# Optimization experiments

Hardware: AMD Instinct MI355X
Metric: run time of the kernel (lower is better)

The kernel has to match this reference:

```python
import jax, jax.numpy as jnp
import numpy as np

EXPERT_NUM = 8
SEQ_LEN = 4096
FREQ_LEN = SEQ_LEN // 2 + 1


def setup_inputs() -> dict:
    key = jax.random.key(0)
    ks = jax.random.split(key, 6)
    B, C = 32, 8
    x = jax.random.normal(ks[0], (B, C, SEQ_LEN), dtype=jnp.float32)
    raw = jax.random.uniform(ks[1], (EXPERT_NUM - 1,), dtype=jnp.float32)
    s1 = 1.0 / np.sqrt(FREQ_LEN)
    W1 = jax.random.uniform(ks[2], (FREQ_LEN, FREQ_LEN), jnp.float32, -s1, s1)
    b1 = jax.random.uniform(ks[3], (FREQ_LEN,), jnp.float32, -s1, s1)
    W2 = jax.random.uniform(ks[4], (EXPERT_NUM, FREQ_LEN), jnp.float32, -s1, s1)
    b2 = jax.random.uniform(ks[5], (EXPERT_NUM,), jnp.float32, -s1, s1)
    return {"x": x, "raw": raw, "W1": W1, "b1": b1, "W2": W2, "b2": b2}


def reference(x, raw, W1, b1, W2, b2):
    # instance norm over seq dim (unbiased variance, like torch.var default)
    x_mean = jnp.mean(x, axis=2, keepdims=True)
    xc = x - x_mean
    n = x.shape[2]
    x_var = jnp.sum(xc * xc, axis=2, keepdims=True) / (n - 1) + 1e-5
    xn = xc / jnp.sqrt(x_var)

    freq_x = jnp.fft.rfft(xn, axis=-1)            # [B, C, F] complex
    F_ = freq_x.shape[-1]

    # sorted sigmoid boundaries -> integer band edges (non-differentiable cast)
    b = jnp.sort(jax.nn.sigmoid(raw))
    boundaries = jnp.concatenate([jnp.zeros(1, x.dtype), b, jnp.ones(1, x.dtype)])
    idx = jnp.floor(jax.lax.stop_gradient(boundaries) * F_).astype(jnp.int32)
    idx = idx.at[-1].set(F_)

    # band-pass masks for all experts at once: [E, F]
    fpos = jnp.arange(F_)
    mask = (fpos[None, :] >= idx[:-1, None]) & (fpos[None, :] < idx[1:, None])

    # per-expert frequency components: [B, E, C, F]
    comp = freq_x[:, None, :, :] * mask[None, :, None, :].astype(freq_x.dtype)
    expert_outputs = jnp.fft.irfft(comp, n=SEQ_LEN, axis=-1)  # [B, E, C, L]

    # gating on channel-averaged magnitude spectrum
    gating_input = jnp.mean(jnp.abs(freq_x), axis=1)          # [B, F]
    h = jax.nn.relu(gating_input @ W1.T + b1)
    gating_scores = jax.nn.softmax(h @ W2.T + b2, axis=-1)    # [B, E]

    # gated combine in frequency domain, then single iFFT
    gate_c = gating_scores.astype(freq_x.dtype)
    combined_freq = jnp.einsum('becf,be->bcf', comp, gate_c)
    combined = jnp.fft.irfft(combined_freq, n=SEQ_LEN, axis=-1)
    combined = combined * jnp.sqrt(x_var) + x_mean
    return combined, boundaries, gating_scores, expert_outputs
```

## Files before the change

kernel.cpp:

```cpp
#include <hip/hip_runtime.h>
#include <hip/hip_bf16.h>


using cplx = float2;
typedef float nfloat2 __attribute__((ext_vector_type(2)));

static constexpr int BB = 32, CCH = 8, LL = 4096, FF = 2049, EE = 8;

static constexpr size_t WS_FREQ  = 0;
static constexpr size_t WS_MEAN  = WS_FREQ + (size_t)BB * CCH * FF * 2;
static constexpr size_t WS_SIGMA = WS_MEAN + 256;
static constexpr size_t WS_GI    = WS_SIGMA + 256;
static constexpr size_t WS_H     = WS_GI + (size_t)BB * FF;
static constexpr size_t WS_IDX   = WS_H + (size_t)BB * FF;
static constexpr size_t WS_EOF   = WS_IDX + 16;
static constexpr size_t WS_LOGIT = WS_EOF + 2049;
static constexpr size_t WS_W2048 = WS_LOGIT + 256;
static constexpr size_t WS_U     = WS_W2048 + 4096;

static constexpr size_t OUT_COMB = 0;
static constexpr size_t OUT_BND  = (size_t)BB * CCH * LL;
static constexpr size_t OUT_GATE = OUT_BND + 9;
static constexpr size_t OUT_EXP  = OUT_GATE + (size_t)BB * EE;

#define PHI(i) ((i) + ((i) >> 5))
__device__ __forceinline__ int scat(int n) {
  return ((n & 3) << 9) | (((n >> 2) & 7) << 6) | (((n >> 5) & 7) << 3) | (n >> 8);
}

template <bool INV>
__device__ __forceinline__ void dft8(float* zr, float* zi) {
  const float C = 0.70710678118654752f;
  float s0r = zr[0] + zr[4], s0i = zi[0] + zi[4];
  float d0r = zr[0] - zr[4], d0i = zi[0] - zi[4];
  float s1r = zr[2] + zr[6], s1i = zi[2] + zi[6];
  float d1r = zr[2] - zr[6], d1i = zi[2] - zi[6];
  float E0r = s0r + s1r, E0i = s0i + s1i;
  float E2r = s0r - s1r, E2i = s0i - s1i;
  float E1r, E1i, E3r, E3i;
  if (!INV) { E1r = d0r + d1i; E1i = d0i - d1r; E3r = d0r - d1i; E3i = d0i + d1r; }
  else      { E1r = d0r - d1i; E1i = d0i + d1r; E3r = d0r + d1i; E3i = d0i - d1r; }
  float t0r = zr[1] + zr[5], t0i = zi[1] + zi[5];
  float e0r = zr[1] - zr[5], e0i = zi[1] - zi[5];
  float t1r = zr[3] + zr[7], t1i = zi[3] + zi[7];
  float e1r = zr[3] - zr[7], e1i = zi[3] - zi[7];
  float O0r = t0r + t1r, O0i = t0i + t1i;
  float O2r = t0r - t1r, O2i = t0i - t1i;
  float O1r, O1i, O3r, O3i;
  if (!INV) { O1r = e0r + e1i; O1i = e0i - e1r; O3r = e0r - e1i; O3i = e0i + e1r; }
  else      { O1r = e0r - e1i; O1i = e0i + e1r; O3r = e0r + e1i; O3i = e0i - e1r; }
  float w1r, w1i, w2r, w2i, w3r, w3i;
  if (!INV) {
    w1r = C * (O1r + O1i); w1i = C * (O1i - O1r);
    w2r = O2i;             w2i = -O2r;
    w3r = C * (O3i - O3r); w3i = -C * (O3r + O3i);
  } else {
    w1r = C * (O1r - O1i); w1i = C * (O1i + O1r);
    w2r = -O2i;            w2i = O2r;
    w3r = -C * (O3r + O3i); w3i = C * (O3r - O3i);
  }
  zr[0] = E0r + O0r; zi[0] = E0i + O0i;
  zr[4] = E0r - O0r; zi[4] = E0i - O0i;
  zr[1] = E1r + w1r; zi[1] = E1i + w1i;
  zr[5] = E1r - w1r; zi[5] = E1i - w1i;
  zr[2] = E2r + w2r; zi[2] = E2i + w2i;
  zr[6] = E2r - w2r; zi[6] = E2i - w2i;
  zr[3] = E3r + w3r; zi[3] = E3i + w3i;
  zr[7] = E3r - w3r; zi[7] = E3i - w3i;
}

template <bool INV>
__device__ __forceinline__ void dft4(float* zr, float* zi) {
  float s0r = zr[0] + zr[2], s0i = zi[0] + zi[2];
  float d0r = zr[0] - zr[2], d0i = zi[0] - zi[2];
  float s1r = zr[1] + zr[3], s1i = zi[1] + zi[3];
  float d1r = zr[1] - zr[3], d1i = zi[1] - zi[3];
  zr[0] = s0r + s1r; zi[0] = s0i + s1i;
  zr[2] = s0r - s1r; zi[2] = s0i - s1i;
  if (!INV) { zr[1] = d0r + d1i; zi[1] = d0i - d1r; zr[3] = d0r - d1i; zi[3] = d0i + d1r; }
  else      { zr[1] = d0r - d1i; zi[1] = d0i + d1r; zr[3] = d0r + d1i; zi[3] = d0i - d1r; }
}

template <bool INV>
__device__ void fftr8(float* ZR, float* ZI, const cplx* __restrict__ W, int t) {
  float zr[8], zi[8];
  {
    int base = 8 * t;
#pragma unroll
    for (int m = 0; m < 8; ++m) { int i = PHI(base + m); zr[m] = ZR[i]; zi[m] = ZI[i]; }
    dft8<INV>(zr, zi);
#pragma unroll
    for (int m = 0; m < 8; ++m) { int i = PHI(base + m); ZR[i] = zr[m]; ZI[i] = zi[m]; }
  }
  __syncthreads();
  {
    int g = t & 31, p = t >> 5;
    int base = 64 * g + p;
#pragma unroll
    for (int m = 0; m < 8; ++m) { int i = PHI(base + 8 * m); zr[m] = ZR[i]; zi[m] = ZI[i]; }
#pragma unroll
    for (int m = 1; m < 8; ++m) {
      cplx w = W[32 * m * p];
      float wi = INV ? -w.y : w.y;
      float xr = zr[m] * w.x - zi[m] * wi;
      float xi = zr[m] * wi + zi[m] * w.x;
      zr[m] = xr; zi[m] = xi;
    }
    dft8<INV>(zr, zi);
#pragma unroll
    for (int m = 0; m < 8; ++m) { int i = PHI(base + 8 * m); ZR[i] = zr[m]; ZI[i] = zi[m]; }
  }
  __syncthreads();
  {
    int g = t & 3, p = t >> 2;
    int base = 512 * g + p;
#pragma unroll
    for (int m = 0; m < 8; ++m) { int i = PHI(base + 64 * m); zr[m] = ZR[i]; zi[m] = ZI[i]; }
#pragma unroll
    for (int m = 1; m < 8; ++m) {
      cplx w = W[4 * m * p];
      float wi = INV ? -w.y : w.y;
      float xr = zr[m] * w.x - zi[m] * wi;
      float xi = zr[m] * wi + zi[m] * w.x;
      zr[m] = xr; zi[m] = xi;
    }
    dft8<INV>(zr, zi);
#pragma unroll
    for (int m = 0; m < 8; ++m) { int i = PHI(base + 64 * m); ZR[i] = zr[m]; ZI[i] = zi[m]; }
  }
  __syncthreads();
  {
#pragma unroll
    for (int h = 0; h < 2; ++h) {
      int p = t + (h << 8);
      float yr[4], yi[4];
#pragma unroll
      for (int m = 0; m < 4; ++m) { int i = PHI(p + 512 * m); yr[m] = ZR[i]; yi[m] = ZI[i]; }
#pragma unroll
      for (int m = 1; m < 4; ++m) {
        cplx w = W[m * p];
        float wi = INV ? -w.y : w.y;
        float xr = yr[m] * w.x - yi[m] * wi;
        float xi = yr[m] * wi + yi[m] * w.x;
        yr[m] = xr; yi[m] = xi;
      }
      dft4<INV>(yr, yi);
#pragma unroll
      for (int m = 0; m < 4; ++m) { int i = PHI(p + 512 * m); ZR[i] = yr[m]; ZI[i] = yi[m]; }
    }
  }
  __syncthreads();
}

__global__ void k_misc(const float* __restrict__ raw,
                       float* __restrict__ out,
                       float* __restrict__ ws) {
  const int blk = blockIdx.x, t = threadIdx.x;
  if (blk < 8) {
    int j = blk * 256 + t;
    float sn, cs;
    sincosf(-6.283185307179586f * (float)j / 2048.0f, &sn, &cs);
    ((cplx*)(ws + WS_W2048))[j] = make_float2(cs, sn);
  } else if (blk < 17) {
    int k = (blk - 8) * 256 + t;
    if (k < FF) {
      float sn, cs;
      sincosf(-3.14159265358979323846f * (float)k / 2048.0f, &sn, &cs);
      ((cplx*)(ws + WS_U))[k] = make_float2(cs, sn);
    }
  } else if (blk == 17) {
    __shared__ int idx_s[9];
    if (t == 0) {
      float v[7];
      for (int i = 0; i < 7; ++i) v[i] = 1.0f / (1.0f + expf(-raw[i]));
      for (int a = 1; a < 7; ++a) {
        float key = v[a];
        int q = a - 1;
        while (q >= 0 && v[q] > key) { v[q + 1] = v[q]; --q; }
        v[q + 1] = key;
      }
      float bnd[9];
      bnd[0] = 0.0f; bnd[8] = 1.0f;
      for (int i = 0; i < 7; ++i) bnd[i + 1] = v[i];
      int* wi = (int*)(ws + WS_IDX);
      for (int e = 0; e < 9; ++e) {
        int id = (int)floorf(bnd[e] * (float)FF);
        if (e == 8) id = FF;
        idx_s[e] = id;
        wi[e] = id;
        out[OUT_BND + e] = bnd[e];
      }
    }
    if (t < 256) {
      ws[WS_LOGIT + t] = 0.f;
    }
    __syncthreads();
    int* eof = (int*)(ws + WS_EOF);
    for (int f = t; f < FF; f += 256) {
      int e = 0;
      for (int q = 1; q < 8; ++q)
        if (f >= idx_s[q]) e = q;
      eof[f] = e;
    }
  } else {
    float4* p = (float4*)(ws + WS_GI);
    const float4 z4 = make_float4(0.f, 0.f, 0.f, 0.f);
    for (int i = (blk - 18) * 256 + t; i < 32784; i += 32 * 256) p[i] = z4;
  }
}

__global__ __launch_bounds__(256) void k_fwd(const float* __restrict__ x,
                                             float* __restrict__ ws) {
  __shared__ float ZR[2112], ZI[2112];
  __shared__ float red[8];
  const int t  = threadIdx.x;
  const int bc = blockIdx.x;
  const int b  = bc >> 3;
  const int lane = t & 63, wid = t >> 6;
  const cplx* W = (const cplx*)(ws + WS_W2048);
  const cplx* U = (const cplx*)(ws + WS_U);
  const float2* xp2 = (const float2*)(x + (size_t)bc * LL);

  float2 v[8];
  float sum = 0.f;
#pragma unroll
  for (int u = 0; u < 8; ++u) {
    v[u] = xp2[t + (u << 8)];
    sum += v[u].x + v[u].y;
  }
#pragma unroll
  for (int off = 32; off > 0; off >>= 1) sum += __shfl_down(sum, off, 64);
  if (lane == 0) red[wid] = sum;
  __syncthreads();
  const float mean = (red[0] + red[1] + red[2] + red[3]) * (1.0f / 4096.0f);

  float ss = 0.f;
#pragma unroll
  for (int u = 0; u < 8; ++u) {
    float dx = v[u].x - mean, dy = v[u].y - mean;
    ss += dx * dx + dy * dy;
  }
#pragma unroll
  for (int off = 32; off > 0; off >>= 1) ss += __shfl_down(ss, off, 64);
  if (lane == 0) red[4 + wid] = ss;
  __syncthreads();
  const float var   = (red[4] + red[5] + red[6] + red[7]) / 4095.0f + 1e-5f;
  const float sigma = sqrtf(var);
  const float inv   = 1.0f / sigma;
  if (t == 0) {
    ws[WS_MEAN + bc]  = mean;
    ws[WS_SIGMA + bc] = sigma;
  }

#pragma unroll
  for (int u = 0; u < 8; ++u) {
    int n = t + (u << 8);
    int i = PHI(scat(n));
    ZR[i] = (v[u].x - mean) * inv;
    ZI[i] = (v[u].y - mean) * inv;
  }
  __syncthreads();

  fftr8<false>(ZR, ZI, W, t);

  cplx* freq = (cplx*)ws + (size_t)bc * FF;
#pragma unroll
  for (int u = 0; u < 9; ++u) {
    int k = t + (u << 8);
    if (k > 2048) break;
    int ka = k & 2047, km = (2048 - k) & 2047;
    float Zkr = ZR[PHI(ka)], Zki = ZI[PHI(ka)];
    float Zmr = ZR[PHI(km)], Zmi = ZI[PHI(km)];
    float fex = 0.5f * (Zkr + Zmr);
    float fey = 0.5f * (Zki - Zmi);
    float fox = 0.5f * (Zki + Zmi);
    float foy = -0.5f * (Zkr - Zmr);
    cplx uk = U[k];
    float rx = fex + uk.x * fox - uk.y * foy;
    float ry = fey + uk.x * foy + uk.y * fox;
    freq[k] = make_float2(rx, ry);
    atomicAdd(&ws[WS_GI + (size_t)b * FF + k], 0.125f * sqrtf(rx * rx + ry * ry));
  }
}

__global__ __launch_bounds__(256) void k_h(const float* __restrict__ W1,
                                           float* __restrict__ ws) {
  __shared__ float W1s[64][33];
  __shared__ float gis[32][33];
  const int t  = threadIdx.x;
  const int i0 = blockIdx.x * 64;
  const int il = t & 63, bg = t >> 6;
  float acc[8] = {0, 0, 0, 0, 0, 0, 0, 0};

  const int fbeg = blockIdx.y * 64;
  const int fend = min(fbeg + 64, FF);
  for (int f0 = fbeg; f0 < fend; f0 += 32) {
    for (int q = t; q < 64 * 32; q += 256) {
      int r = q >> 5, cc = q & 31;
      int gi_i = i0 + r, gf = f0 + cc;
      W1s[r][cc] = (gi_i < FF && gf < FF) ? W1[(size_t)gi_i * FF + gf] : 0.f;
    }
    for (int q = t; q < 32 * 32; q += 256) {
      int bb = q >> 5, cc = q & 31;
      int gf = f0 + cc;
      gis[bb][cc] = (gf < FF) ? ws[WS_GI + (size_t)bb * FF + gf] : 0.f;
    }
    __syncthreads();
#pragma unroll 8
    for (int cc = 0; cc < 32; ++cc) {
      float wv = W1s[il][cc];
#pragma unroll
      for (int j = 0; j < 8; ++j) acc[j] += wv * gis[bg * 8 + j][cc];
    }
    __syncthreads();
  }
  int ii = i0 + il;
  if (ii < FF) {
#pragma unroll
    for (int j = 0; j < 8; ++j)
      atomicAdd(&ws[WS_H + (size_t)(bg * 8 + j) * FF + ii], acc[j]);
  }
}

__global__ __launch_bounds__(256) void k_logits1(const float* __restrict__ b1,
                                                 const float* __restrict__ W2,
                                                 float* __restrict__ ws) {
  const int b = blockIdx.x, kc = blockIdx.y, t = threadIdx.x;
  const int kbeg = kc * 257, kend = min(kbeg + 257, FF);
  float p[8] = {0, 0, 0, 0, 0, 0, 0, 0};
  for (int f = kbeg + t; f < kend; f += 256) {
    float hv = fmaxf(ws[WS_H + (size_t)b * FF + f] + b1[f], 0.f);
#pragma unroll
    for (int e = 0; e < 8; ++e) p[e] += hv * W2[(size_t)e * FF + f];
  }
#pragma unroll
  for (int off = 32; off > 0; off >>= 1) {
#pragma unroll
    for (int e = 0; e < 8; ++e) p[e] += __shfl_down(p[e], off, 64);
  }
  __shared__ float red[4][8];
  const int lane = t & 63, wid = t >> 6;
  if (lane == 0) {
#pragma unroll
    for (int e = 0; e < 8; ++e) red[wid][e] = p[e];
  }
  __syncthreads();
  if (t < 8)
    atomicAdd(&ws[WS_LOGIT + (size_t)b * 8 + t],
              red[0][t] + red[1][t] + red[2][t] + red[3][t]);
}

__global__ __launch_bounds__(256) void k_ifft(const float* __restrict__ b2,
                                              const float* __restrict__ ws,
                                              float* __restrict__ out) {
  __shared__ float ZR[2112], ZI[2112];
  __shared__ float lg[8];
  __shared__ float gates_s[8];
  __shared__ int   lohi[2];
  const int t   = threadIdx.x;
  const int blk = blockIdx.x;
  const int j   = blk % 9;
  const int bc  = blk / 9;
  const int b   = bc >> 3, c = bc & 7;
  const bool comb = (j == 8);

  const cplx* freq = (const cplx*)ws + (size_t)bc * FF;
  const int*  idxp = (const int*)(ws + WS_IDX);
  const int*  eof  = (const int*)(ws + WS_EOF);
  const cplx* W    = (const cplx*)(ws + WS_W2048);
  const cplx* U    = (const cplx*)(ws + WS_U);

  if (t < 8) lg[t] = ws[WS_LOGIT + (size_t)b * 8 + t] + b2[t];
  if (t == 0) {
    lohi[0] = comb ? 0 : idxp[j];
    lohi[1] = comb ? FF : idxp[j + 1];
  }
  __syncthreads();
  const int lo = lohi[0], hi = lohi[1];

  if (comb) {
    if (t < 8) {
      float mx = lg[0];
#pragma unroll
      for (int q = 1; q < 8; ++q) mx = fmaxf(mx, lg[q]);
      float sm = 0.f;
#pragma unroll
      for (int q = 0; q < 8; ++q) sm += expf(lg[q] - mx);
      float g = expf(lg[t] - mx) / sm;
      gates_s[t] = g;
      if (c == 0) out[OUT_GATE + (size_t)b * 8 + t] = g;
    }
    __syncthreads();
  }

#pragma unroll
  for (int u = 0; u < 8; ++u) {
    int k  = t + (u << 8);
    int km = 2048 - k;
    cplx A = make_float2(0.f, 0.f), Bv = make_float2(0.f, 0.f);
    if (comb) {
      A  = freq[k];
      Bv = freq[km];
      float gk = gates_s[eof[k]], gm = gates_s[eof[km]];
      A.x *= gk; A.y *= gk; Bv.x *= gm; Bv.y *= gm;
    } else {
      if (k >= lo && k < hi)   A  = freq[k];
      if (km >= lo && km < hi) Bv = freq[km];
    }
    float Px = A.x - Bv.x, Py = A.y + Bv.y;
    float Qx = A.x + Bv.x, Qy = A.y - Bv.y;
    cplx uk = U[k];
    float cs = uk.x, sn = -uk.y;
    float Xox = 0.5f * (cs * Px - sn * Py);
    float Xoy = 0.5f * (cs * Py + sn * Px);
    int i = PHI(scat(k));
    ZR[i] = 0.5f * Qx - Xoy;
    ZI[i] = 0.5f * Qy + Xox;
  }
  __syncthreads();

  fftr8<true>(ZR, ZI, W, t);

  if (comb) {
    const float mul = ws[WS_SIGMA + bc] * (1.0f / 2048.0f);
    const float add = ws[WS_MEAN + bc];
    nfloat2* op = (nfloat2*)(out + OUT_COMB + (size_t)bc * LL);
#pragma unroll
    for (int u = 0; u < 8; ++u) {
      int n = t + (u << 8);
      nfloat2 o;
      o.x = ZR[PHI(n)] * mul + add;
      o.y = ZI[PHI(n)] * mul + add;
      __builtin_nontemporal_store(o, op + n);
    }
  } else {
    const float mul = 1.0f / 2048.0f;
    float* op = out + OUT_EXP + (((size_t)(b * EE + j) * CCH + c) * LL);
    if (t == 0) __builtin_nontemporal_store(ZR[PHI(0)] * mul, op);
#pragma unroll
    for (int u = 0; u < 8; ++u) {
      int n = t + (u << 8);
      if (n < 2047) {
        nfloat2 o;
        o.x = ZI[PHI(n)] * mul;
        o.y = ZR[PHI(n + 1)] * mul;
        __builtin_nontemporal_store(o, (nfloat2*)(op + 2 * n + 1));
      } else {
        __builtin_nontemporal_store(ZI[PHI(2047)] * mul, op + 4095);
      }
    }
  }
}

extern "C" void kernel_launch(void* const* d_in, const int* in_sizes, int n_in,
                              void* d_out, int out_size, void* d_ws, size_t ws_size,
                              hipStream_t stream) {
  const float* x   = (const float*)d_in[0];
  const float* raw = (const float*)d_in[1];
  const float* W1  = (const float*)d_in[2];
  const float* b1  = (const float*)d_in[3];
  const float* W2  = (const float*)d_in[4];
  const float* b2  = (const float*)d_in[5];
  float* out = (float*)d_out;
  float* ws  = (float*)d_ws;

  k_misc<<<50, 256, 0, stream>>>(raw, out, ws);
  k_fwd<<<BB * CCH, 256, 0, stream>>>(x, ws);
  k_h<<<dim3(33, 33), 256, 0, stream>>>(W1, ws);
  k_logits1<<<dim3(BB, 8), 256, 0, stream>>>(b1, W2, ws);
  k_ifft<<<BB * CCH * 9, 256, 0, stream>>>(b2, ws, out);
}
```

Measured before the change: 140.0 us.

## Co-schedule W1 GEMM with expert iFFTs and fuse logits into combined iFFT

Merges the W1 gating GEMM and the 2048 per-expert iFFT blocks into one launch, since the expert iFFTs do not depend on the gating result, so the two can share the GPU. The logits reduction, softmax and combined iFFT move into a separate final kernel in which each block recomputes its batch's full W2 dot product, replacing the atomic logits buffer and one launch. Expert blocks are remapped so each bc is pinned to one XCD slot, aiming at better L2 reuse of the frequency data. The cost is redundant logits work in every block of the same batch, plus 7 idle blocks in the merged launch.

```diff
diff --git a/kernel.cpp b/kernel.cpp
--- a/kernel.cpp
+++ b/kernel.cpp
@@ -191,9 +191,6 @@
         out[OUT_BND + e] = bnd[e];
       }
     }
-    if (t < 256) {
-      ws[WS_LOGIT + t] = 0.f;
-    }
     __syncthreads();
     int* eof = (int*)(ws + WS_EOF);
     for (int f = t; f < FF; f += 256) {
@@ -283,130 +280,71 @@
   }
 }
 
-__global__ __launch_bounds__(256) void k_h(const float* __restrict__ W1,
-                                           float* __restrict__ ws) {
-  __shared__ float W1s[64][33];
-  __shared__ float gis[32][33];
-  const int t  = threadIdx.x;
-  const int i0 = blockIdx.x * 64;
-  const int il = t & 63, bg = t >> 6;
-  float acc[8] = {0, 0, 0, 0, 0, 0, 0, 0};
-
-  const int fbeg = blockIdx.y * 64;
-  const int fend = min(fbeg + 64, FF);
-  for (int f0 = fbeg; f0 < fend; f0 += 32) {
-    for (int q = t; q < 64 * 32; q += 256) {
-      int r = q >> 5, cc = q & 31;
-      int gi_i = i0 + r, gf = f0 + cc;
-      W1s[r][cc] = (gi_i < FF && gf < FF) ? W1[(size_t)gi_i * FF + gf] : 0.f;
-    }
-    for (int q = t; q < 32 * 32; q += 256) {
-      int bb = q >> 5, cc = q & 31;
-      int gf = f0 + cc;
-      gis[bb][cc] = (gf < FF) ? ws[WS_GI + (size_t)bb * FF + gf] : 0.f;
-    }
-    __syncthreads();
+__global__ __launch_bounds__(256) void k_mid(const float* __restrict__ W1,
+                                             float* __restrict__ ws,
+                                             float* __restrict__ out) {
+  __shared__ float SM[4224];
+  const int p = blockIdx.x, t = threadIdx.x;
+
+  if (p < 1089) {
+    float* W1s = SM;
+    float* gis = SM + 2112;
+    const int i0 = (p % 33) * 64;
+    const int il = t & 63, bg = t >> 6;
+    float acc[8] = {0, 0, 0, 0, 0, 0, 0, 0};
+    const int fbeg = (p / 33) * 64;
+    const int fend = min(fbeg + 64, FF);
+    for (int f0 = fbeg; f0 < fend; f0 += 32) {
+      for (int q = t; q < 64 * 32; q += 256) {
+        int r = q >> 5, cc = q & 31;
+        int gi_i = i0 + r, gf = f0 + cc;
+        W1s[r * 33 + cc] = (gi_i < FF && gf < FF) ? W1[(size_t)gi_i * FF + gf] : 0.f;
+      }
+      for (int q = t; q < 32 * 32; q += 256) {
+        int bb = q >> 5, cc = q & 31;
+        int gf = f0 + cc;
+        gis[bb * 33 + cc] = (gf < FF) ? ws[WS_GI + (size_t)bb * FF + gf] : 0.f;
+      }
+      __syncthreads();
 #pragma unroll 8
-    for (int cc = 0; cc < 32; ++cc) {
-      float wv = W1s[il][cc];
-#pragma unroll
-      for (int j = 0; j < 8; ++j) acc[j] += wv * gis[bg * 8 + j][cc];
-    }
-    __syncthreads();
-  }
-  int ii = i0 + il;
-  if (ii < FF) {
-#pragma unroll
-    for (int j = 0; j < 8; ++j)
-      atomicAdd(&ws[WS_H + (size_t)(bg * 8 + j) * FF + ii], acc[j]);
-  }
-}
-
-__global__ __launch_bounds__(256) void k_logits1(const float* __restrict__ b1,
-                                                 const float* __restrict__ W2,
-                                                 float* __restrict__ ws) {
-  const int b = blockIdx.x, kc = blockIdx.y, t = threadIdx.x;
-  const int kbeg = kc * 257, kend = min(kbeg + 257, FF);
-  float p[8] = {0, 0, 0, 0, 0, 0, 0, 0};
-  for (int f = kbeg + t; f < kend; f += 256) {
-    float hv = fmaxf(ws[WS_H + (size_t)b * FF + f] + b1[f], 0.f);
-#pragma unroll
-    for (int e = 0; e < 8; ++e) p[e] += hv * W2[(size_t)e * FF + f];
-  }
-#pragma unroll
-  for (int off = 32; off > 0; off >>= 1) {
-#pragma unroll
-    for (int e = 0; e < 8; ++e) p[e] += __shfl_down(p[e], off, 64);
-  }
-  __shared__ float red[4][8];
-  const int lane = t & 63, wid = t >> 6;
-  if (lane == 0) {
-#pragma unroll
-    for (int e = 0; e < 8; ++e) red[wid][e] = p[e];
-  }
-  __syncthreads();
-  if (t < 8)
-    atomicAdd(&ws[WS_LOGIT + (size_t)b * 8 + t],
-              red[0][t] + red[1][t] + red[2][t] + red[3][t]);
-}
-
-__global__ __launch_bounds__(256) void k_ifft(const float* __restrict__ b2,
-                                              const float* __restrict__ ws,
-                                              float* __restrict__ out) {
-  __shared__ float ZR[2112], ZI[2112];
-  __shared__ float lg[8];
-  __shared__ float gates_s[8];
-  __shared__ int   lohi[2];
-  const int t   = threadIdx.x;
-  const int blk = blockIdx.x;
-  const int j   = blk % 9;
-  const int bc  = blk / 9;
+      for (int cc = 0; cc < 32; ++cc) {
+        float wv = W1s[il * 33 + cc];
+#pragma unroll
+        for (int j = 0; j < 8; ++j) acc[j] += wv * gis[(bg * 8 + j) * 33 + cc];
+      }
+      __syncthreads();
+    }
+    int ii = i0 + il;
+    if (ii < FF) {
+#pragma unroll
+      for (int j = 0; j < 8; ++j)
+        atomicAdd(&ws[WS_H + (size_t)(bg * 8 + j) * FF + ii], acc[j]);
+    }
+    return;
+  }
+  if (p < 1096) return;
+
+  const int e9  = p - 1096;
+  const int xcd = e9 & 7, slot = e9 >> 3;
+  const int bc  = ((slot >> 3) << 3) | xcd;
+  const int j   = slot & 7;
   const int b   = bc >> 3, c = bc & 7;
-  const bool comb = (j == 8);
-
+
+  float* ZR = SM;
+  float* ZI = SM + 2112;
   const cplx* freq = (const cplx*)ws + (size_t)bc * FF;
   const int*  idxp = (const int*)(ws + WS_IDX);
-  const int*  eof  = (const int*)(ws + WS_EOF);
   const cplx* W    = (const cplx*)(ws + WS_W2048);
   const cplx* U    = (const cplx*)(ws + WS_U);
-
-  if (t < 8) lg[t] = ws[WS_LOGIT + (size_t)b * 8 + t] + b2[t];
-  if (t == 0) {
-    lohi[0] = comb ? 0 : idxp[j];
-    lohi[1] = comb ? FF : idxp[j + 1];
-  }
-  __syncthreads();
-  const int lo = lohi[0], hi = lohi[1];
-
-  if (comb) {
-    if (t < 8) {
-      float mx = lg[0];
-#pragma unroll
-      for (int q = 1; q < 8; ++q) mx = fmaxf(mx, lg[q]);
-      float sm = 0.f;
-#pragma unroll
-      for (int q = 0; q < 8; ++q) sm += expf(lg[q] - mx);
-      float g = expf(lg[t] - mx) / sm;
-      gates_s[t] = g;
-      if (c == 0) out[OUT_GATE + (size_t)b * 8 + t] = g;
-    }
-    __syncthreads();
-  }
+  const int lo = idxp[j], hi = idxp[j + 1];
 
 #pragma unroll
   for (int u = 0; u < 8; ++u) {
     int k  = t + (u << 8);
     int km = 2048 - k;
     cplx A = make_float2(0.f, 0.f), Bv = make_float2(0.f, 0.f);
-    if (comb) {
-      A  = freq[k];
-      Bv = freq[km];
-      float gk = gates_s[eof[k]], gm = gates_s[eof[km]];
-      A.x *= gk; A.y *= gk; Bv.x *= gm; Bv.y *= gm;
-    } else {
-      if (k >= lo && k < hi)   A  = freq[k];
-      if (km >= lo && km < hi) Bv = freq[km];
-    }
+    if (k >= lo && k < hi)   A  = freq[k];
+    if (km >= lo && km < hi) Bv = freq[km];
     float Px = A.x - Bv.x, Py = A.y + Bv.y;
     float Qx = A.x + Bv.x, Qy = A.y - Bv.y;
     cplx uk = U[k];
@@ -421,34 +359,106 @@
 
   fftr8<true>(ZR, ZI, W, t);
 
-  if (comb) {
-    const float mul = ws[WS_SIGMA + bc] * (1.0f / 2048.0f);
-    const float add = ws[WS_MEAN + bc];
-    nfloat2* op = (nfloat2*)(out + OUT_COMB + (size_t)bc * LL);
-#pragma unroll
-    for (int u = 0; u < 8; ++u) {
-      int n = t + (u << 8);
+  const float mul = 1.0f / 2048.0f;
+  float* op = out + OUT_EXP + (((size_t)(b * EE + j) * CCH + c) * LL);
+  if (t == 0) __builtin_nontemporal_store(ZR[PHI(0)] * mul, op);
+#pragma unroll
+  for (int u = 0; u < 8; ++u) {
+    int n = t + (u << 8);
+    if (n < 2047) {
       nfloat2 o;
-      o.x = ZR[PHI(n)] * mul + add;
-      o.y = ZI[PHI(n)] * mul + add;
-      __builtin_nontemporal_store(o, op + n);
-    }
-  } else {
-    const float mul = 1.0f / 2048.0f;
-    float* op = out + OUT_EXP + (((size_t)(b * EE + j) * CCH + c) * LL);
-    if (t == 0) __builtin_nontemporal_store(ZR[PHI(0)] * mul, op);
-#pragma unroll
-    for (int u = 0; u < 8; ++u) {
-      int n = t + (u << 8);
-      if (n < 2047) {
-        nfloat2 o;
-        o.x = ZI[PHI(n)] * mul;
-        o.y = ZR[PHI(n + 1)] * mul;
-        __builtin_nontemporal_store(o, (nfloat2*)(op + 2 * n + 1));
-      } else {
-        __builtin_nontemporal_store(ZI[PHI(2047)] * mul, op + 4095);
-      }
-    }
+      o.x = ZI[PHI(n)] * mul;
+      o.y = ZR[PHI(n + 1)] * mul;
+      __builtin_nontemporal_store(o, (nfloat2*)(op + 2 * n + 1));
+    } else {
+      __builtin_nontemporal_store(ZI[PHI(2047)] * mul, op + 4095);
+    }
+  }
+}
+
+__global__ __launch_bounds__(256) void k_comb(const float* __restrict__ b1,
+                                              const float* __restrict__ W2,
+                                              const float* __restrict__ b2,
+                                              const float* __restrict__ ws,
+                                              float* __restrict__ out) {
+  __shared__ float ZR[2112], ZI[2112];
+  __shared__ float red[4][8];
+  __shared__ float lg[8];
+  __shared__ float gates_s[8];
+  const int t  = threadIdx.x;
+  const int bc = blockIdx.x;
+  const int b  = bc >> 3, c = bc & 7;
+  const int lane = t & 63, wid = t >> 6;
+
+  float pacc[8] = {0, 0, 0, 0, 0, 0, 0, 0};
+  const float* hrow = ws + WS_H + (size_t)b * FF;
+  for (int f = t; f < FF; f += 256) {
+    float hv = fmaxf(hrow[f] + b1[f], 0.f);
+#pragma unroll
+    for (int e = 0; e < 8; ++e) pacc[e] += hv * W2[(size_t)e * FF + f];
+  }
+#pragma unroll
+  for (int off = 32; off > 0; off >>= 1) {
+#pragma unroll
+    for (int e = 0; e < 8; ++e) pacc[e] += __shfl_down(pacc[e], off, 64);
+  }
+  if (lane == 0) {
+#pragma unroll
+    for (int e = 0; e < 8; ++e) red[wid][e] = pacc[e];
+  }
+  __syncthreads();
+  if (t < 8) lg[t] = red[0][t] + red[1][t] + red[2][t] + red[3][t] + b2[t];
+  __syncthreads();
+  if (t < 8) {
+    float mx = lg[0];
+#pragma unroll
+    for (int q = 1; q < 8; ++q) mx = fmaxf(mx, lg[q]);
+    float sm = 0.f;
+#pragma unroll
+    for (int q = 0; q < 8; ++q) sm += expf(lg[q] - mx);
+    float g = expf(lg[t] - mx) / sm;
+    gates_s[t] = g;
+    if (c == 0) out[OUT_GATE + (size_t)b * 8 + t] = g;
+  }
+  __syncthreads();
+
+  const cplx* freq = (const cplx*)ws + (size_t)bc * FF;
+  const int*  eof  = (const int*)(ws + WS_EOF);
+  const cplx* W    = (const cplx*)(ws + WS_W2048);
+  const cplx* U    = (const cplx*)(ws + WS_U);
+
+#pragma unroll
+  for (int u = 0; u < 8; ++u) {
+    int k  = t + (u << 8);
+    int km = 2048 - k;
+    cplx A  = freq[k];
+    cplx Bv = freq[km];
+    float gk = gates_s[eof[k]], gm = gates_s[eof[km]];
+    A.x *= gk; A.y *= gk; Bv.x *= gm; Bv.y *= gm;
+    float Px = A.x - Bv.x, Py = A.y + Bv.y;
+    float Qx = A.x + Bv.x, Qy = A.y - Bv.y;
+    cplx uk = U[k];
+    float cs = uk.x, sn = -uk.y;
+    float Xox = 0.5f * (cs * Px - sn * Py);
+    float Xoy = 0.5f * (cs * Py + sn * Px);
+    int i = PHI(scat(k));
+    ZR[i] = 0.5f * Qx - Xoy;
+    ZI[i] = 0.5f * Qy + Xox;
+  }
+  __syncthreads();
+
+  fftr8<true>(ZR, ZI, W, t);
+
+  const float mul = ws[WS_SIGMA + bc] * (1.0f / 2048.0f);
+  const float add = ws[WS_MEAN + bc];
+  nfloat2* op = (nfloat2*)(out + OUT_COMB + (size_t)bc * LL);
+#pragma unroll
+  for (int u = 0; u < 8; ++u) {
+    int n = t + (u << 8);
+    nfloat2 o;
+    o.x = ZR[PHI(n)] * mul + add;
+    o.y = ZI[PHI(n)] * mul + add;
+    __builtin_nontemporal_store(o, op + n);
   }
 }
 
@@ -466,7 +476,6 @@
 
   k_misc<<<50, 256, 0, stream>>>(raw, out, ws);
   k_fwd<<<BB * CCH, 256, 0, stream>>>(x, ws);
-  k_h<<<dim3(33, 33), 256, 0, stream>>>(W1, ws);
-  k_logits1<<<dim3(BB, 8), 256, 0, stream>>>(b1, W2, ws);
-  k_ifft<<<BB * CCH * 9, 256, 0, stream>>>(b2, ws, out);
-}
+  k_mid<<<1096 + 2048, 256, 0, stream>>>(W1, ws, out);
+  k_comb<<<BB * CCH, 256, 0, stream>>>(b1, W2, b2, ws, out);
+}
```

Result: faster. 134.8 us (-3.7%).
